# Kernel optimization log

Hardware: AMD Instinct MI355X
Metric: run time of the kernel (lower is better)

The kernel has to match this reference:

```python
import jax, jax.numpy as jnp
import numpy as np

D_MODEL, D_K, D_FF, N = 1024, 128, 4096, 8192

def _linear_params(key, fan_in, fan_out):
    # mimic torch nn.Linear default init (uniform +/- 1/sqrt(fan_in))
    k1, k2 = jax.random.split(key)
    bound = 1.0 / np.sqrt(fan_in)
    W = jax.random.uniform(k1, (fan_out, fan_in), jnp.float32, -bound, bound)
    b = jax.random.uniform(k2, (fan_out,), jnp.float32, -bound, bound)
    return W, b

def setup_inputs() -> dict:
    key = jax.random.key(0)
    ks = jax.random.split(key, 7)
    x = jax.random.normal(ks[0], (N, D_MODEL), jnp.float32)
    Wq, bq = _linear_params(ks[1], D_MODEL, D_K)
    Wk, bk = _linear_params(ks[2], D_MODEL, D_K)
    Wv, bv = _linear_params(ks[3], D_MODEL, D_K)
    Wp, bp = _linear_params(ks[4], D_K, D_MODEL)
    W1, b1 = _linear_params(ks[5], D_MODEL, D_FF)
    W2, b2 = _linear_params(ks[6], D_FF, D_MODEL)
    return {"x": x, "Wq": Wq, "bq": bq, "Wk": Wk, "bk": bk, "Wv": Wv, "bv": bv,
            "Wp": Wp, "bp": bp, "W1": W1, "b1": b1, "W2": W2, "b2": b2}

def reference(x, Wq, bq, Wk, bk, Wv, bv, Wp, bp, W1, b1, W2, b2):
    # projections (torch Linear: x @ W.T + b)
    Q = x @ Wq.T + bq            # [n, d_k]
    K = x @ Wk.T + bk            # [n, d_k]
    V = x @ Wv.T + bv            # [n, d_k]
    # linear attention, original evaluation order: (Q @ K^T) @ V
    attn = Q @ K.T               # [n, n]
    context = attn @ V           # [n, d_k]
    out = context @ Wp.T + bp    # [n, d_model]
    x = x + out                  # residual 1
    h = jax.nn.relu(x @ W1.T + b1)  # [n, d_ff]
    return x + (h @ W2.T + b2)   # residual 2
```

## Files before the change

### kernel.cpp

```cpp
#include <hip/hip_runtime.h>


#define MROWS 8192
#define DMODEL 1024
#define DK 128
#define DFF 4096

typedef __attribute__((ext_vector_type(8))) __bf16 bf16x8;
typedef __attribute__((ext_vector_type(4))) float f32x4;

#define BAR()     __builtin_amdgcn_s_barrier()
#define WAITV(n)  asm volatile("s_waitcnt vmcnt(" #n ")" ::: "memory")
#define LGKMC(n)  asm volatile("s_waitcnt lgkmcnt(" #n ")" ::: "memory")
#define SCHED0()  __builtin_amdgcn_sched_barrier(0)
#define GLOAD(src, dst) __builtin_amdgcn_global_load_lds( \
    (const __attribute__((address_space(1))) void*)(src), \
    (__attribute__((address_space(3))) void*)(dst), 16, 0, 0)

#define LDSO(p) ((unsigned)(unsigned long long) \
    (__attribute__((address_space(3))) const char*)(const char*)(p))

__device__ __forceinline__ bf16x8 ldsr(unsigned off) {
    bf16x8 r;
    asm volatile("ds_read_b128 %0, %1" : "=v"(r) : "v"(off));
    return r;
}

__device__ __forceinline__ void cast_one(const float* s, __bf16* d, int i) {
    const float4 a = reinterpret_cast<const float4*>(s)[2 * i];
    const float4 b = reinterpret_cast<const float4*>(s)[2 * i + 1];
    bf16x8 o;
    o[0] = (__bf16)a.x; o[1] = (__bf16)a.y; o[2] = (__bf16)a.z; o[3] = (__bf16)a.w;
    o[4] = (__bf16)b.x; o[5] = (__bf16)b.y; o[6] = (__bf16)b.z; o[7] = (__bf16)b.w;
    reinterpret_cast<bf16x8*>(d)[i] = o;
}

__global__ __launch_bounds__(256) void cast6b(
    const float* __restrict__ s0, __bf16* __restrict__ d0,
    const float* __restrict__ s1, __bf16* __restrict__ d1,
    const float* __restrict__ s2, __bf16* __restrict__ d2,
    const float* __restrict__ s3, __bf16* __restrict__ d3,
    const float* __restrict__ s4, __bf16* __restrict__ d4,
    const float* __restrict__ s5, __bf16* __restrict__ d5,
    const float* __restrict__ ba, const float* __restrict__ bb,
    const float* __restrict__ bc, float* __restrict__ bo)
{
    const int b = blockIdx.x, t = threadIdx.x;
    if      (b <  64)  cast_one(s0, d0, b * 256 + t);
    else if (b < 128)  cast_one(s1, d1, (b - 64) * 256 + t);
    else if (b < 192)  cast_one(s2, d2, (b - 128) * 256 + t);
    else if (b < 256)  cast_one(s3, d3, (b - 192) * 256 + t);
    else if (b < 2304) cast_one(s4, d4, (b - 256) * 256 + t);
    else if (b < 4352) cast_one(s5, d5, (b - 2304) * 256 + t);
    else if (t < 128) { bo[t] = ba[t]; bo[128 + t] = bb[t]; bo[256 + t] = bc[t]; }
}

__global__ __launch_bounds__(256) void ffn2_reduce2(
    float* __restrict__ y, const __bf16* __restrict__ x2b,
    const __bf16* __restrict__ P0, const __bf16* __restrict__ P1,
    const float* __restrict__ b2, int n8)
{
    for (int i = blockIdx.x * blockDim.x + threadIdx.x; i < n8;
         i += gridDim.x * blockDim.x) {
        const int col0 = (i << 3) & (DMODEL - 1);
        const float4 ba = *reinterpret_cast<const float4*>(&b2[col0]);
        const float4 bb = *reinterpret_cast<const float4*>(&b2[col0 + 4]);
        const bf16x8 xx = reinterpret_cast<const bf16x8*>(x2b)[i];
        const bf16x8 p0 = reinterpret_cast<const bf16x8*>(P0)[i];
        const bf16x8 p1 = reinterpret_cast<const bf16x8*>(P1)[i];
        float4 o0, o1;
        o0.x = (float)xx[0] + (float)p0[0] + (float)p1[0] + ba.x;
        o0.y = (float)xx[1] + (float)p0[1] + (float)p1[1] + ba.y;
        o0.z = (float)xx[2] + (float)p0[2] + (float)p1[2] + ba.z;
        o0.w = (float)xx[3] + (float)p0[3] + (float)p1[3] + ba.w;
        o1.x = (float)xx[4] + (float)p0[4] + (float)p1[4] + bb.x;
        o1.y = (float)xx[5] + (float)p0[5] + (float)p1[5] + bb.y;
        o1.z = (float)xx[6] + (float)p0[6] + (float)p1[6] + bb.z;
        o1.w = (float)xx[7] + (float)p0[7] + (float)p1[7] + bb.w;
        reinterpret_cast<float4*>(y)[2 * i]     = o0;
        reinterpret_cast<float4*>(y)[2 * i + 1] = o1;
    }
}

template<bool RELU, bool RESID, bool BIAS, bool OUTBF, bool DUAL, bool F32A>
__global__ __launch_bounds__(256) void gemm128(
    const void* __restrict__ Ap, int lda,
    const __bf16* __restrict__ W,
    const float* __restrict__ bias,
    const float* __restrict__ resid,
    void* __restrict__ Cout, __bf16* __restrict__ Cbf, int ldc, int K)
{
    constexpr int BK = 32;
    __shared__ __bf16 As[128 * BK];
    __shared__ __bf16 Bs[128 * BK];

    const int tid  = threadIdx.x;
    const int lane = tid & 63;
    const int w    = tid >> 6;
    const int wm   = w >> 1;
    const int wn   = w & 1;
    const int fr   = lane & 15;
    const int fq   = lane >> 4;

    const long row0 = (long)blockIdx.y * 128;
    const long col0 = (long)blockIdx.x * 128;

    const int sr = (w << 4) + (lane >> 2);
    const int sc = (lane & 3) << 3;

    const __bf16* gA0 = F32A ? nullptr : (const __bf16*)Ap + (row0 + sr) * (long)lda + sc;
    const __bf16* gA1 = F32A ? nullptr : (const __bf16*)Ap + (row0 + 64 + sr) * (long)lda + sc;
    const float*  gAf = F32A ? (const float*)Ap + (row0 + (tid >> 1)) * (long)lda
                               + ((tid & 1) << 4)
                             : nullptr;
    const __bf16* gW0 = W + (col0 + sr) * (long)K + sc;
    const __bf16* gW1 = W + (col0 + 64 + sr) * (long)K + sc;

    __bf16* lA0 = &As[(w << 4) * BK];
    __bf16* lA1 = &As[((w << 4) + 64) * BK];
    __bf16* lB0 = &Bs[(w << 4) * BK];
    __bf16* lB1 = &Bs[((w << 4) + 64) * BK];

    f32x4 acc[4][4] = {};

    for (int k0 = 0; k0 < K; k0 += BK) {
        if constexpr (F32A) {
            const float* s = gAf + k0;
            const float4 f0 = reinterpret_cast<const float4*>(s)[0];
            const float4 f1 = reinterpret_cast<const float4*>(s)[1];
            const float4 f2 = reinterpret_cast<const float4*>(s)[2];
            const float4 f3 = reinterpret_cast<const float4*>(s)[3];
            bf16x8 o0, o1;
            o0[0] = (__bf16)f0.x; o0[1] = (__bf16)f0.y; o0[2] = (__bf16)f0.z; o0[3] = (__bf16)f0.w;
            o0[4] = (__bf16)f1.x; o0[5] = (__bf16)f1.y; o0[6] = (__bf16)f1.z; o0[7] = (__bf16)f1.w;
            o1[0] = (__bf16)f2.x; o1[1] = (__bf16)f2.y; o1[2] = (__bf16)f2.z; o1[3] = (__bf16)f2.w;
            o1[4] = (__bf16)f3.x; o1[5] = (__bf16)f3.y; o1[6] = (__bf16)f3.z; o1[7] = (__bf16)f3.w;
            const int ar = tid >> 1, ac = (tid & 1) << 4;
            *reinterpret_cast<bf16x8*>(&As[ar * BK + ac])     = o0;
            *reinterpret_cast<bf16x8*>(&As[ar * BK + ac + 8]) = o1;
        } else {
            GLOAD(gA0 + k0, lA0);
            GLOAD(gA1 + k0, lA1);
        }
        GLOAD(gW0 + k0, lB0);
        GLOAD(gW1 + k0, lB1);
        __syncthreads();

        bf16x8 af[4], bfr[4];
        #pragma unroll
        for (int m = 0; m < 4; m++)
            af[m] = *reinterpret_cast<const bf16x8*>(
                &As[(wm * 64 + m * 16 + fr) * BK + fq * 8]);
        #pragma unroll
        for (int n = 0; n < 4; n++)
            bfr[n] = *reinterpret_cast<const bf16x8*>(
                &Bs[(wn * 64 + n * 16 + fr) * BK + fq * 8]);

        #pragma unroll
        for (int m = 0; m < 4; m++)
            #pragma unroll
            for (int n = 0; n < 4; n++)
                acc[m][n] = __builtin_amdgcn_mfma_f32_16x16x32_bf16(
                    af[m], bfr[n], acc[m][n], 0, 0, 0);
        __syncthreads();
    }

    float bc[4];
    #pragma unroll
    for (int n = 0; n < 4; n++)
        bc[n] = BIAS ? bias[col0 + wn * 64 + n * 16 + fr] : 0.0f;
    #pragma unroll
    for (int m = 0; m < 4; m++) {
        #pragma unroll
        for (int j = 0; j < 4; j++) {
            const long r = row0 + wm * 64 + m * 16 + fq * 4 + j;
            #pragma unroll
            for (int n = 0; n < 4; n++) {
                const long c = col0 + wn * 64 + n * 16 + fr;
                float v = acc[m][n][j] + bc[n];
                if constexpr (RESID) v += resid[r * ldc + c];
                if constexpr (RELU)  v = fmaxf(v, 0.0f);
                if constexpr (OUTBF) ((__bf16*)Cout)[r * ldc + c] = (__bf16)v;
                else                 ((float*)Cout)[r * ldc + c] = v;
                if constexpr (DUAL)  Cbf[r * ldc + c] = (__bf16)v;
            }
        }
    }
}

#define RD_B()                                             \
    _Pragma("unroll")                                      \
    for (int n = 0; n < 4; n++) {                          \
        bb[n][0] = ldsr(pB + rb0 + n * 2048);              \
        bb[n][1] = ldsr(pB + rb1 + n * 2048);              \
    }
#define RD_A(m0_, cnt_)                                    \
    _Pragma("unroll")                                      \
    for (int m = m0_; m < m0_ + cnt_; m++) {               \
        a[m][0] = ldsr(pA + rb0 + m * 2048);               \
        a[m][1] = ldsr(pA + rb1 + m * 2048);               \
    }
#define MFMA2(m0_)                                                            \
    _Pragma("unroll")                                                         \
    for (int m = m0_; m < m0_ + 2; m++)                                       \
        _Pragma("unroll")                                                     \
        for (int n = 0; n < 4; n++) {                                         \
            acc[m][n] = __builtin_amdgcn_mfma_f32_16x16x32_bf16(              \
                a[m][0], bb[n][0], acc[m][n], 0, 0, 0);                       \
            acc[m][n] = __builtin_amdgcn_mfma_f32_16x16x32_bf16(              \
                a[m][1], bb[n][1], acc[m][n], 0, 0, 0);                       \
        }

template<bool RELU, bool BIAS>
__global__ __launch_bounds__(256, 2) void gemm256x128(
    const __bf16* __restrict__ A, int lda,
    const __bf16* __restrict__ W, int ldw,
    const float* __restrict__ bias,
    __bf16* __restrict__ Cout, long sstride, int ldc,
    int klen, int nb, int nbx)
{
    __shared__ char lds[49152];

    const int bid = blockIdx.x;
    const int sid = bid / nb;
    const int ib  = bid % nb;
    const int chunk = nb >> 3;
    const int swz   = (ib & 7) * chunk + (ib >> 3);
    const int bx    = swz % nbx;
    const int by    = swz / nbx;

    const long row0 = (long)by * 256;
    const long col0 = (long)bx * 128;

    const __bf16* Ash = A + (long)sid * klen;
    const __bf16* Wsh = W + (long)sid * klen;

    const int tid  = threadIdx.x;
    const int lane = tid & 63;
    const int w    = tid >> 6;
    const int wm   = w >> 1;
    const int wn   = w & 1;
    const int fr   = lane & 15;
    const int fq   = lane >> 4;

    const int scole = ((lane & 7) ^ (lane >> 3)) << 3;
    const __bf16* gA = Ash + (row0 + w * 8 + (lane >> 3)) * (long)lda + scole;
    const __bf16* gB = Wsh + (col0 + w * 8 + (lane >> 3)) * (long)ldw + scole;

    char* ldsc = &lds[0];
    const unsigned lbase = LDSO(ldsc);
    const int nt = klen >> 6;

    auto stage = [&](int t) {
        const __bf16* ap = gA + (long)t * 64;
        const __bf16* bp = gB + (long)t * 64;
        #pragma unroll
        for (int r = 0; r < 8; r++)
            GLOAD(ap + (long)(32 * r) * lda, ldsc + r * 4096 + (w << 10));
        #pragma unroll
        for (int r = 0; r < 4; r++)
            GLOAD(bp + (long)(32 * r) * ldw, ldsc + 32768 + r * 4096 + (w << 10));
    };

    const unsigned rb0 = fr * 128 + ((fq * 16) ^ ((fr & 7) << 4));
    const unsigned rb1 = fr * 128 + ((64 + fq * 16) ^ ((fr & 7) << 4));
    const unsigned pA = lbase + (wm << 14);
    const unsigned pB = lbase + 32768 + (wn << 13);

    f32x4 acc[8][4] = {};
    bf16x8 a[8][2], bb[4][2];

    for (int t = 0; t < nt; ++t) {
        stage(t);
        WAITV(0);
        BAR();

        RD_B();
        RD_A(0, 8);

        LGKMC(12); SCHED0();
        __builtin_amdgcn_s_setprio(1); MFMA2(0); __builtin_amdgcn_s_setprio(0);
        LGKMC(8); SCHED0();
        __builtin_amdgcn_s_setprio(1); MFMA2(2); __builtin_amdgcn_s_setprio(0);
        LGKMC(4); SCHED0();
        __builtin_amdgcn_s_setprio(1); MFMA2(4); __builtin_amdgcn_s_setprio(0);
        LGKMC(0); SCHED0();
        __builtin_amdgcn_s_setprio(1); MFMA2(6); __builtin_amdgcn_s_setprio(0);

        BAR();
    }

    __bf16* Cb = Cout + (long)sid * sstride;
    float bc[4];
    #pragma unroll
    for (int n = 0; n < 4; n++)
        bc[n] = BIAS ? bias[col0 + wn * 64 + n * 16 + fr] : 0.0f;

    __bf16* sw = reinterpret_cast<__bf16*>(ldsc) + (w << 12);
    const long crow0 = row0 + wm * 128;
    const long ccol0 = col0 + wn * 64;
    #pragma unroll
    for (int half = 0; half < 2; half++) {
        #pragma unroll
        for (int m = 0; m < 4; m++)
            #pragma unroll
            for (int j = 0; j < 4; j++) {
                const int row = m * 16 + fq * 4 + j;
                #pragma unroll
                for (int n = 0; n < 4; n++) {
                    float v = acc[half * 4 + m][n][j] + bc[n];
                    if constexpr (RELU) v = fmaxf(v, 0.0f);
                    sw[row * 64 + n * 16 + fr] = (__bf16)v;
                }
            }
        #pragma unroll
        for (int i = 0; i < 8; i++) {
            const bf16x8 vv = *reinterpret_cast<const bf16x8*>(sw + i * 512 + lane * 8);
            const int r  = half * 64 + i * 8 + (lane >> 3);
            const int cg = (lane & 7) << 3;
            *reinterpret_cast<bf16x8*>(&Cb[(crow0 + r) * (long)ldc + ccol0 + cg]) = vv;
        }
        __builtin_amdgcn_s_waitcnt(0);
    }
}

__global__ __launch_bounds__(256) void ktv_partial(
    const __bf16* __restrict__ Kp, const __bf16* __restrict__ Vp,
    int ld, float* __restrict__ part)
{
    __shared__ float ks[32][DK];
    __shared__ float vs[32][DK];
    const int tid = threadIdx.x;
    const int ti  = tid >> 4;
    const int tj  = tid & 15;
    float acc[8][8] = {};
    const long base = (long)blockIdx.x * 128;

    for (int n0 = 0; n0 < 128; n0 += 32) {
        for (int t = tid; t < 512; t += 256) {
            const int r  = t >> 4;
            const int cc = (t & 15) << 3;
            const bf16x8 k8 = *reinterpret_cast<const bf16x8*>(
                &Kp[(base + n0 + r) * (long)ld + cc]);
            const bf16x8 v8 = *reinterpret_cast<const bf16x8*>(
                &Vp[(base + n0 + r) * (long)ld + cc]);
            #pragma unroll
            for (int u = 0; u < 8; u++) {
                ks[r][cc + u] = (float)k8[u];
                vs[r][cc + u] = (float)v8[u];
            }
        }
        __syncthreads();
        for (int n = 0; n < 32; n++) {
            float kk[8], vv[8];
            #pragma unroll
            for (int i = 0; i < 8; i++) kk[i] = ks[n][(ti << 3) + i];
            #pragma unroll
            for (int j = 0; j < 8; j++) vv[j] = vs[n][(tj << 3) + j];
            #pragma unroll
            for (int i = 0; i < 8; i++)
                #pragma unroll
                for (int j = 0; j < 8; j++)
                    acc[i][j] = fmaf(kk[i], vv[j], acc[i][j]);
        }
        __syncthreads();
    }

    float* dst = &part[(long)blockIdx.x * (DK * DK)];
    #pragma unroll
    for (int i = 0; i < 8; i++) {
        const int ig = (ti << 3) + i;
        *reinterpret_cast<float4*>(&dst[ig * DK + (tj << 3)]) =
            make_float4(acc[i][0], acc[i][1], acc[i][2], acc[i][3]);
        *reinterpret_cast<float4*>(&dst[ig * DK + (tj << 3) + 4]) =
            make_float4(acc[i][4], acc[i][5], acc[i][6], acc[i][7]);
    }
}

__global__ __launch_bounds__(256) void ktv_reduce(
    const float* __restrict__ part, __bf16* __restrict__ ktvR)
{
    const int t = blockIdx.x * 256 + threadIdx.x;
    float s = 0.0f;
    for (int b = 0; b < 64; b++) s += part[(long)b * (DK * DK) + t];
    ktvR[t] = (__bf16)s;
}

extern "C" void kernel_launch(void* const* d_in, const int* in_sizes, int n_in,
                              void* d_out, int out_size, void* d_ws, size_t ws_size,
                              hipStream_t stream) {
    const float* x  = (const float*)d_in[0];
    const float* Wq = (const float*)d_in[1];
    const float* bq = (const float*)d_in[2];
    const float* Wk = (const float*)d_in[3];
    const float* bk = (const float*)d_in[4];
    const float* Wv = (const float*)d_in[5];
    const float* bv = (const float*)d_in[6];
    const float* Wp = (const float*)d_in[7];
    const float* bp = (const float*)d_in[8];
    const float* W1 = (const float*)d_in[9];
    const float* b1 = (const float*)d_in[10];
    const float* W2 = (const float*)d_in[11];
    const float* b2 = (const float*)d_in[12];
    float* out = (float*)d_out;

    char* ws = (char*)d_ws;
    const size_t MB = 1ull << 20;
    __bf16* P0b   = (__bf16*)(ws);
    __bf16* P1b   = P0b + (long)MROWS * DMODEL;
    __bf16* x2b   = (__bf16*)(ws +  34 * MB);
    __bf16* Hb    = (__bf16*)(ws +  51 * MB);
    __bf16* QKVb  = (__bf16*)(ws + 119 * MB);
    __bf16* W1b   = (__bf16*)(ws + 126 * MB);
    __bf16* W2b   = (__bf16*)(ws + 135 * MB);
    __bf16* Wqkvb = (__bf16*)(ws + 144 * MB);
    __bf16* Wpb   = (__bf16*)(ws + 145 * MB);
    float*  Part  = (float*) (ws + 146 * MB);
    __bf16* KtvRb = (__bf16*)(ws + 151 * MB);
    __bf16* MtB   = (__bf16*)(ws + 152 * MB);
    float*  bqkvf = (float*) (ws + 155 * MB);

    const dim3 blk(256);

    cast6b<<<4353, blk, 0, stream>>>(
        Wq, Wqkvb, Wk, Wqkvb + DK * DMODEL, Wv, Wqkvb + 2 * DK * DMODEL,
        Wp, Wpb, W1, W1b, W2, W2b, bq, bk, bv, bqkvf);

    gemm128<false,false,true,true,false,true><<<dim3(3, 64), blk, 0, stream>>>(
        x, DMODEL, Wqkvb, bqkvf, nullptr, QKVb, nullptr, 3 * DK, DMODEL);

    ktv_partial<<<64, blk, 0, stream>>>(QKVb + DK, QKVb + 2 * DK, 3 * DK, Part);
    ktv_reduce <<<64, blk, 0, stream>>>(Part, KtvRb);

    gemm128<false,false,false,true,false,false><<<dim3(1, 8), blk, 0, stream>>>(
        Wpb, DK, KtvRb, nullptr, nullptr, MtB, nullptr, DK, DK);

    gemm128<false,true,true,true,false,false><<<dim3(8, 64), blk, 0, stream>>>(
        QKVb, 3 * DK, MtB, bp, x, x2b, nullptr, DMODEL, DK);

    gemm256x128<true,true><<<1024, blk, 0, stream>>>(
        x2b, DMODEL, W1b, DMODEL, b1, Hb, 0, DFF, DMODEL, 1024, DFF / 128);

    gemm256x128<false,false><<<512, blk, 0, stream>>>(
        Hb, DFF, W2b, DFF, nullptr, P0b,
        (long)MROWS * DMODEL, DMODEL, DFF / 2, 256, DMODEL / 128);

    ffn2_reduce2<<<2048, blk, 0, stream>>>(out, x2b, P0b, P1b, b2,
                                           MROWS * DMODEL / 8);
}
```

Before: 221.6 us.

## Shrink FFN GEMM tiles to 128x128 with K=32 steps for higher occupancy

Replaces the 256x128 FFN GEMM kernel with a 128x128-tile kernel that stages 32-wide K slices in 16 KB of LDS, uses a new XOR swizzle, and raises launch bounds to 3 blocks per CU. Grid sizes double for both FFN GEMMs. The aim is more resident waves and better latency hiding. In exchange, arithmetic intensity per tile drops, and the shorter K step means twice as many barriers and global-load waits per unit of work, with no double buffering.

```diff
diff --git a/kernel.cpp b/kernel.cpp
--- a/kernel.cpp
+++ b/kernel.cpp
@@ -188,38 +188,15 @@
     }
 }
 
-#define RD_B()                                             \
-    _Pragma("unroll")                                      \
-    for (int n = 0; n < 4; n++) {                          \
-        bb[n][0] = ldsr(pB + rb0 + n * 2048);              \
-        bb[n][1] = ldsr(pB + rb1 + n * 2048);              \
-    }
-#define RD_A(m0_, cnt_)                                    \
-    _Pragma("unroll")                                      \
-    for (int m = m0_; m < m0_ + cnt_; m++) {               \
-        a[m][0] = ldsr(pA + rb0 + m * 2048);               \
-        a[m][1] = ldsr(pA + rb1 + m * 2048);               \
-    }
-#define MFMA2(m0_)                                                            \
-    _Pragma("unroll")                                                         \
-    for (int m = m0_; m < m0_ + 2; m++)                                       \
-        _Pragma("unroll")                                                     \
-        for (int n = 0; n < 4; n++) {                                         \
-            acc[m][n] = __builtin_amdgcn_mfma_f32_16x16x32_bf16(              \
-                a[m][0], bb[n][0], acc[m][n], 0, 0, 0);                       \
-            acc[m][n] = __builtin_amdgcn_mfma_f32_16x16x32_bf16(              \
-                a[m][1], bb[n][1], acc[m][n], 0, 0, 0);                       \
-        }
-
 template<bool RELU, bool BIAS>
-__global__ __launch_bounds__(256, 2) void gemm256x128(
+__global__ __launch_bounds__(256, 3) void gemm_ffn128(
     const __bf16* __restrict__ A, int lda,
     const __bf16* __restrict__ W, int ldw,
     const float* __restrict__ bias,
     __bf16* __restrict__ Cout, long sstride, int ldc,
     int klen, int nb, int nbx)
 {
-    __shared__ char lds[49152];
+    __shared__ char lds[16384];
 
     const int bid = blockIdx.x;
     const int sid = bid / nb;
@@ -229,7 +206,7 @@
     const int bx    = swz % nbx;
     const int by    = swz / nbx;
 
-    const long row0 = (long)by * 256;
+    const long row0 = (long)by * 128;
     const long col0 = (long)bx * 128;
 
     const __bf16* Ash = A + (long)sid * klen;
@@ -243,49 +220,61 @@
     const int fr   = lane & 15;
     const int fq   = lane >> 4;
 
-    const int scole = ((lane & 7) ^ (lane >> 3)) << 3;
-    const __bf16* gA = Ash + (row0 + w * 8 + (lane >> 3)) * (long)lda + scole;
-    const __bf16* gB = Wsh + (col0 + w * 8 + (lane >> 3)) * (long)ldw + scole;
+    const int sr = (w << 4) + (lane >> 2);
+    const int sc = (((lane & 3) ^ ((lane >> 3) & 3)) << 3);
+    const __bf16* gA0 = Ash + (row0 + sr) * (long)lda + sc;
+    const __bf16* gA1 = Ash + (row0 + 64 + sr) * (long)lda + sc;
+    const __bf16* gW0 = Wsh + (col0 + sr) * (long)ldw + sc;
+    const __bf16* gW1 = Wsh + (col0 + 64 + sr) * (long)ldw + sc;
 
     char* ldsc = &lds[0];
     const unsigned lbase = LDSO(ldsc);
-    const int nt = klen >> 6;
-
-    auto stage = [&](int t) {
-        const __bf16* ap = gA + (long)t * 64;
-        const __bf16* bp = gB + (long)t * 64;
-        #pragma unroll
-        for (int r = 0; r < 8; r++)
-            GLOAD(ap + (long)(32 * r) * lda, ldsc + r * 4096 + (w << 10));
-        #pragma unroll
-        for (int r = 0; r < 4; r++)
-            GLOAD(bp + (long)(32 * r) * ldw, ldsc + 32768 + r * 4096 + (w << 10));
-    };
-
-    const unsigned rb0 = fr * 128 + ((fq * 16) ^ ((fr & 7) << 4));
-    const unsigned rb1 = fr * 128 + ((64 + fq * 16) ^ ((fr & 7) << 4));
-    const unsigned pA = lbase + (wm << 14);
-    const unsigned pB = lbase + 32768 + (wn << 13);
-
-    f32x4 acc[8][4] = {};
-    bf16x8 a[8][2], bb[4][2];
+    const int nt = klen >> 5;
+
+    char* lA0 = ldsc + (w << 10);
+    char* lA1 = ldsc + 4096  + (w << 10);
+    char* lB0 = ldsc + 8192  + (w << 10);
+    char* lB1 = ldsc + 12288 + (w << 10);
+
+    const unsigned rb = fr * 64 + ((fq ^ ((fr >> 1) & 3)) << 4);
+    const unsigned pA = lbase + (wm << 12);
+    const unsigned pB = lbase + 8192 + (wn << 12);
+
+    f32x4 acc[4][4] = {};
+    bf16x8 af[4], bfr[4];
 
     for (int t = 0; t < nt; ++t) {
-        stage(t);
+        const long k0 = (long)t * 32;
+        GLOAD(gA0 + k0, lA0);
+        GLOAD(gA1 + k0, lA1);
+        GLOAD(gW0 + k0, lB0);
+        GLOAD(gW1 + k0, lB1);
         WAITV(0);
         BAR();
 
-        RD_B();
-        RD_A(0, 8);
-
-        LGKMC(12); SCHED0();
-        __builtin_amdgcn_s_setprio(1); MFMA2(0); __builtin_amdgcn_s_setprio(0);
-        LGKMC(8); SCHED0();
-        __builtin_amdgcn_s_setprio(1); MFMA2(2); __builtin_amdgcn_s_setprio(0);
-        LGKMC(4); SCHED0();
-        __builtin_amdgcn_s_setprio(1); MFMA2(4); __builtin_amdgcn_s_setprio(0);
+        #pragma unroll
+        for (int n = 0; n < 4; n++) bfr[n] = ldsr(pB + rb + n * 1024);
+        #pragma unroll
+        for (int m = 0; m < 4; m++) af[m]  = ldsr(pA + rb + m * 1024);
+
+        LGKMC(2); SCHED0();
+        __builtin_amdgcn_s_setprio(1);
+        #pragma unroll
+        for (int m = 0; m < 2; m++)
+            #pragma unroll
+            for (int n = 0; n < 4; n++)
+                acc[m][n] = __builtin_amdgcn_mfma_f32_16x16x32_bf16(
+                    af[m], bfr[n], acc[m][n], 0, 0, 0);
+        __builtin_amdgcn_s_setprio(0);
         LGKMC(0); SCHED0();
-        __builtin_amdgcn_s_setprio(1); MFMA2(6); __builtin_amdgcn_s_setprio(0);
+        __builtin_amdgcn_s_setprio(1);
+        #pragma unroll
+        for (int m = 2; m < 4; m++)
+            #pragma unroll
+            for (int n = 0; n < 4; n++)
+                acc[m][n] = __builtin_amdgcn_mfma_f32_16x16x32_bf16(
+                    af[m], bfr[n], acc[m][n], 0, 0, 0);
+        __builtin_amdgcn_s_setprio(0);
 
         BAR();
     }
@@ -296,27 +285,29 @@
     for (int n = 0; n < 4; n++)
         bc[n] = BIAS ? bias[col0 + wn * 64 + n * 16 + fr] : 0.0f;
 
-    __bf16* sw = reinterpret_cast<__bf16*>(ldsc) + (w << 12);
-    const long crow0 = row0 + wm * 128;
+    __bf16* sw = reinterpret_cast<__bf16*>(ldsc) + (w << 11);
+    const long crow0 = row0 + wm * 64;
     const long ccol0 = col0 + wn * 64;
     #pragma unroll
-    for (int half = 0; half < 2; half++) {
-        #pragma unroll
-        for (int m = 0; m < 4; m++)
+    for (int pass = 0; pass < 2; pass++) {
+        #pragma unroll
+        for (int mi = 0; mi < 2; mi++) {
+            const int m = pass * 2 + mi;
             #pragma unroll
             for (int j = 0; j < 4; j++) {
-                const int row = m * 16 + fq * 4 + j;
+                const int row = mi * 16 + fq * 4 + j;
                 #pragma unroll
                 for (int n = 0; n < 4; n++) {
-                    float v = acc[half * 4 + m][n][j] + bc[n];
+                    float v = acc[m][n][j] + bc[n];
                     if constexpr (RELU) v = fmaxf(v, 0.0f);
                     sw[row * 64 + n * 16 + fr] = (__bf16)v;
                 }
             }
-        #pragma unroll
-        for (int i = 0; i < 8; i++) {
+        }
+        #pragma unroll
+        for (int i = 0; i < 4; i++) {
             const bf16x8 vv = *reinterpret_cast<const bf16x8*>(sw + i * 512 + lane * 8);
-            const int r  = half * 64 + i * 8 + (lane >> 3);
+            const int r  = pass * 32 + i * 8 + (lane >> 3);
             const int cg = (lane & 7) << 3;
             *reinterpret_cast<bf16x8*>(&Cb[(crow0 + r) * (long)ldc + ccol0 + cg]) = vv;
         }
@@ -438,12 +429,12 @@
     gemm128<false,true,true,true,false,false><<<dim3(8, 64), blk, 0, stream>>>(
         QKVb, 3 * DK, MtB, bp, x, x2b, nullptr, DMODEL, DK);
 
-    gemm256x128<true,true><<<1024, blk, 0, stream>>>(
-        x2b, DMODEL, W1b, DMODEL, b1, Hb, 0, DFF, DMODEL, 1024, DFF / 128);
-
-    gemm256x128<false,false><<<512, blk, 0, stream>>>(
+    gemm_ffn128<true,true><<<2048, blk, 0, stream>>>(
+        x2b, DMODEL, W1b, DMODEL, b1, Hb, 0, DFF, DMODEL, 2048, DFF / 128);
+
+    gemm_ffn128<false,false><<<1024, blk, 0, stream>>>(
         Hb, DFF, W2b, DFF, nullptr, P0b,
-        (long)MROWS * DMODEL, DMODEL, DFF / 2, 256, DMODEL / 128);
+        (long)MROWS * DMODEL, DMODEL, DFF / 2, 512, DMODEL / 128);
 
     ffn2_reduce2<<<2048, blk, 0, stream>>>(out, x2b, P0b, P1b, b2,
                                            MROWS * DMODEL / 8);
```

New measurement: 253.9 us. 1.15x slower.
